# Kernel optimization log

Hardware: AMD Instinct MI355X
Metric: run time of the kernel (lower is better)

The kernel has to match this reference:

```python
import jax, jax.numpy as jnp
import numpy as np

VOCAB, INPUT, HIDDEN, OUT = 100000, 256, 512, 5
BATCH, SEQ = 64, 512

def _xavier(key, shape):
    fan_in, fan_out = shape[1], shape[0]
    limit = float(np.sqrt(6.0 / (fan_in + fan_out)))
    return jax.random.uniform(key, shape, jnp.float32, -limit, limit)

def setup_inputs() -> dict:
    key = jax.random.key(0)
    ks = jax.random.split(key, 5)
    x = jax.random.randint(ks[0], (BATCH, SEQ), 0, VOCAB)
    embedding = _xavier(ks[1], (VOCAB, INPUT))
    embedding = embedding.at[0].set(0.0)  # padding_idx=0
    W_ih = _xavier(ks[2], (4 * HIDDEN, INPUT))
    b_ih = jnp.zeros((4 * HIDDEN,), jnp.float32)
    W_hh = _xavier(ks[3], (4 * HIDDEN, HIDDEN))
    b_hh = jnp.zeros((4 * HIDDEN,), jnp.float32)
    W_out = _xavier(ks[4], (OUT, HIDDEN))
    b_out = jnp.zeros((OUT,), jnp.float32)
    return {"x": x, "embedding": embedding, "W_ih": W_ih, "b_ih": b_ih,
            "W_hh": W_hh, "b_hh": b_hh, "W_out": W_out, "b_out": b_out}

def reference(x, embedding, W_ih, b_ih, W_hh, b_hh, W_out, b_out):
    bs = x.shape[0]
    HS = W_hh.shape[1]
    # embedding lookup for all timesteps; padding_idx=0 rows are zero
    emb = embedding[x]                                   # [B, S, INPUT]
    emb = jnp.where((x == 0)[..., None], 0.0, emb)
    # input-to-hidden projection is time-independent: hoist out of the recurrence
    x_proj = jnp.einsum('bsi,gi->bsg', emb, W_ih) + b_ih + b_hh  # [B, S, 4H]

    def step(carry, xp_t):
        h, c = carry
        gates = xp_t + h @ W_hh.T                        # [B, 4H]
        i = jax.nn.sigmoid(gates[:, :HS])
        f = jax.nn.sigmoid(gates[:, HS:2 * HS])
        g = jnp.tanh(gates[:, 2 * HS:3 * HS])
        o = jax.nn.sigmoid(gates[:, 3 * HS:])
        c = f * c + i * g
        h = o * jnp.tanh(c)
        return (h, c), None

    h0 = jnp.zeros((bs, HS), x_proj.dtype)
    c0 = jnp.zeros((bs, HS), x_proj.dtype)
    (h_t, c_t), _ = jax.lax.scan(step, (h0, c0), jnp.swapaxes(x_proj, 0, 1))
    out = h_t @ W_out.T + b_out                          # [B, OUT]
    return out, (h_t, c_t)
```

## Files before the change

kernel.cpp:

```cpp
#include <hip/hip_runtime.h>
#include <stdint.h>

typedef unsigned short u16;
typedef uint32_t u32;
typedef __attribute__((ext_vector_type(4))) u32 u32x4;
typedef __attribute__((ext_vector_type(8))) short v8s;
typedef __attribute__((ext_vector_type(4))) float f32x4;

#define OFF_H  0
#define OFF_WF 262144

__device__ __forceinline__ u16 bf_hi(float v) {
  return (u16)(__builtin_bit_cast(u32, v) >> 16);
}
__device__ __forceinline__ float bf_up(u16 h) {
  return __builtin_bit_cast(float, (u32)h << 16);
}
__device__ __forceinline__ float tanhf_fast(float x) {
  float e = __expf(2.f * x);
  return 1.f - 2.f / (e + 1.f);
}
__device__ __forceinline__ float sigm(float x) {
  return 1.f / (1.f + __expf(-x));
}
__device__ __forceinline__ u32 pkhi(u32 a, u32 b) { return __builtin_amdgcn_perm(b, a, 0x07060302u); }
__device__ __forceinline__ u32 pklo(u32 a, u32 b) { return __builtin_amdgcn_perm(b, a, 0x05040100u); }

__global__ void k_init(u32* h) {
  int i = blockIdx.x * 256 + threadIdx.x;
  if (i < 65536) h[i] = (i < 32768) ? 0u : 1u;
}

__global__ void k_prep(const float* __restrict__ Wih, const float* __restrict__ Whh,
                       u16* __restrict__ wf) {
  int idx = blockIdx.x * 256 + threadIdx.x;
  if (idx >= 64 * 2 * 24 * 64) return;
  int lane = idx & 63;
  int r1 = idx >> 6;
  int c  = r1 % 24;
  int r2 = r1 / 24;
  int nt = r2 & 1;
  int wg = r2 >> 1;
  int n32 = nt * 16 + (lane & 15);
  int R = (n32 >> 3) * 512 + wg * 8 + (n32 & 7);
  int gq = lane >> 4;
  const float* src = (c < 8) ? (Wih + (size_t)R * 256 + c * 32 + 8 * gq)
                             : (Whh + (size_t)R * 512 + (c - 8) * 32 + 8 * gq);
  u16* d = wf + (size_t)idx * 16;
#pragma unroll
  for (int i = 0; i < 8; ++i) {
    float v = src[i];
    u16 hi = bf_hi(v);
    float lo = v - bf_up(hi);
    d[i] = hi;
    d[8 + i] = bf_hi(lo);
  }
}

#define LOADP(DST, PTR) \
  asm volatile("global_load_dwordx4 %0, %1, off" : "=v"(DST) : "v"(PTR))
#define LOADC(DST, PTR) \
  asm volatile("global_load_dwordx4 %0, %1, off sc0 sc1" : "=v"(DST) : "v"(PTR))
#define STORED(PTR, VAL) \
  asm volatile("global_store_dword %0, %1, off sc0 sc1" :: "v"(PTR), "v"(VAL) : "memory")

#define WAITV_(N) { asm volatile("s_waitcnt vmcnt(" #N ")" ::: "memory"); \
                    __builtin_amdgcn_sched_barrier(0); }
#define WAITV(N) WAITV_(N)

#define MFMA16(a, b, c) __builtin_amdgcn_mfma_f32_16x16x32_bf16((a), (b), (c), 0, 0, 0)
#define BC(x) __builtin_bit_cast(v8s, x)

#define MM6(AH, AL, B) { \
  v8s b0h_ = BC((B)[0]), b0l_ = BC((B)[1]), b1h_ = BC((B)[2]), b1l_ = BC((B)[3]); \
  acc[0] = MFMA16((AH), b0h_, acc[0]); \
  acc[0] = MFMA16((AH), b0l_, acc[0]); \
  acc[0] = MFMA16((AL), b0h_, acc[0]); \
  acc[1] = MFMA16((AH), b1h_, acc[1]); \
  acc[1] = MFMA16((AH), b1l_, acc[1]); \
  acc[1] = MFMA16((AL), b1h_, acc[1]); }

#define TAGOK(j) (__all((( (HA[2*(j)][0]^texp) | (HA[2*(j)][1]^texp) \
                         | (HA[2*(j)][2]^texp) | (HA[2*(j)][3]^texp) \
                         | (HA[2*(j)+1][0]^texp) | (HA[2*(j)+1][1]^texp) \
                         | (HA[2*(j)+1][2]^texp) | (HA[2*(j)+1][3]^texp)) & 1u) == 0u))

#define CONSJ(j) { \
  u32x4 w0 = HA[2*(j)], w1 = HA[2*(j)+1]; \
  u32x4 hiw, low; \
  hiw[0] = pkhi(w0[0], w0[1]); hiw[1] = pkhi(w0[2], w0[3]); \
  hiw[2] = pkhi(w1[0], w1[1]); hiw[3] = pkhi(w1[2], w1[3]); \
  low[0] = pklo(w0[0], w0[1]); low[1] = pklo(w0[2], w0[3]); \
  low[2] = pklo(w1[0], w1[1]); low[3] = pklo(w1[2], w1[3]); \
  v8s ah = BC(hiw), al = BC(low); \
  MM6(ah, al, BH[j]); }

#define ISSUEJ(j) { LOADC(HA[2*(j)], pp[j]); LOADC(HA[2*(j)+1], pp[j] + 4); }
#define RISS(c)  if (pend & (1u<<(c))) ISSUEJ(c)
#define RCON(c)  if (pend & (1u<<(c))) { if (TAGOK(c)) { CONSJ(c); pend &= ~(1u<<(c)); } }

__global__ __launch_bounds__(256, 1) void k_lstm(
    const int* __restrict__ xin, const float* __restrict__ emb,
    const float* __restrict__ bih, const float* __restrict__ bhh,
    uint8_t* __restrict__ ws, float* __restrict__ dout)
{
  const int bid = blockIdx.x;
  const int wg = bid & 63;
  const int g  = bid >> 6;
  const int tid = threadIdx.x;
  const int wv = tid >> 6;
  const int lane = tid & 63;
  const int cl = lane & 15;
  const int gq = lane >> 4;

  u32* hbuf = (u32*)(ws + OFF_H);
  const u16* wf = (const u16*)(ws + OFF_WF);

  __shared__ f32x4 red[2][4][2][64];

  float bias[2];
#pragma unroll
  for (int nt = 0; nt < 2; ++nt) {
    int n32 = nt * 16 + cl;
    int R = (n32 >> 3) * 512 + wg * 8 + (n32 & 7);
    bias[nt] = bih[R] + bhh[R];
  }

  u32x4 BH[4][4], WB[2][4];
#pragma unroll
  for (int j = 0; j < 4; ++j) {
    const u32x4* p0 = (const u32x4*)(wf + ((((size_t)wg*2+0)*24 + (8 + wv + 4*j))*64 + lane)*16);
    const u32x4* p1 = (const u32x4*)(wf + ((((size_t)wg*2+1)*24 + (8 + wv + 4*j))*64 + lane)*16);
    BH[j][0] = p0[0]; BH[j][1] = p0[1];
    BH[j][2] = p1[0]; BH[j][3] = p1[1];
  }
#pragma unroll
  for (int J = 0; J < 2; ++J) {
    const u32x4* p0 = (const u32x4*)(wf + ((((size_t)wg*2+0)*24 + (4*J + wv))*64 + lane)*16);
    const u32x4* p1 = (const u32x4*)(wf + ((((size_t)wg*2+1)*24 + (4*J + wv))*64 + lane)*16);
    WB[J][0] = p0[0]; WB[J][1] = p0[1];
    WB[J][2] = p1[0]; WB[J][3] = p1[1];
  }

  const int brow = g * 16 + cl;
  const int koA = wv * 32 + 8 * gq;
  const int koB = (4 + wv) * 32 + 8 * gq;

  u32x4 EA[4];
  {
    int tok0 = xin[brow * 512];
    const float* eb = emb + (size_t)tok0 * 256;
    LOADP(EA[0], eb + koA); LOADP(EA[1], eb + koA + 4);
    LOADP(EA[2], eb + koB); LOADP(EA[3], eb + koB + 4);
  }
  WAITV(0);

  float cst[4] = {0.f, 0.f, 0.f, 0.f};
  int delay = 16;

  for (int t = 0; t < 512; ++t) {
    const u32* hc = hbuf + ((size_t)(t & 1) * 4 + g) * 8192;
    u32* hn = hbuf + ((size_t)((t + 1) & 1) * 4 + g) * 8192;
    const u32 texp = (u32)((t >> 1) & 1);
    const u32* pp[4];
    pp[0] = hc + cl * 512 + (wv + 0) * 32 + 8 * gq;
    pp[1] = hc + cl * 512 + (wv + 4) * 32 + 8 * gq;
    pp[2] = hc + cl * 512 + (wv + 8) * 32 + 8 * gq;
    pp[3] = hc + cl * 512 + (wv + 12) * 32 + 8 * gq;

    for (int d = delay; d > 0; --d) __builtin_amdgcn_s_sleep(1);

    int tok;
    asm volatile("global_load_dword %0, %1, off"
                 : "=v"(tok) : "v"(xin + brow * 512 + ((t + 1) & 511)));
    u32x4 HA[8];
    ISSUEJ(0); ISSUEJ(1); ISSUEJ(2); ISSUEJ(3);
    __builtin_amdgcn_sched_barrier(0);

    WAITV(13);
    f32x4 acc[2] = {};
    {
      u32x4 h0, h1;
      h0[0] = pkhi(EA[0][0], EA[0][1]); h0[1] = pkhi(EA[0][2], EA[0][3]);
      h0[2] = pkhi(EA[1][0], EA[1][1]); h0[3] = pkhi(EA[1][2], EA[1][3]);
      h1[0] = pkhi(EA[2][0], EA[2][1]); h1[1] = pkhi(EA[2][2], EA[2][3]);
      h1[2] = pkhi(EA[3][0], EA[3][1]); h1[3] = pkhi(EA[3][2], EA[3][3]);
      v8s a0 = BC(h0), a1 = BC(h1);
      acc[0] = MFMA16(a0, BC(WB[0][0]), acc[0]);
      acc[0] = MFMA16(a0, BC(WB[0][1]), acc[0]);
      acc[1] = MFMA16(a0, BC(WB[0][2]), acc[1]);
      acc[1] = MFMA16(a0, BC(WB[0][3]), acc[1]);
      acc[0] = MFMA16(a1, BC(WB[1][0]), acc[0]);
      acc[0] = MFMA16(a1, BC(WB[1][1]), acc[0]);
      acc[1] = MFMA16(a1, BC(WB[1][2]), acc[1]);
      acc[1] = MFMA16(a1, BC(WB[1][3]), acc[1]);
    }

    u32 pend = 0;
    WAITV(6); if (TAGOK(0)) { CONSJ(0); } else pend |= 1u;
    WAITV(4); if (TAGOK(1)) { CONSJ(1); } else pend |= 2u;
    WAITV(2); if (TAGOK(2)) { CONSJ(2); } else pend |= 4u;
    WAITV(0); if (TAGOK(3)) { CONSJ(3); } else pend |= 8u;

    delay = pend ? ((delay > 56) ? 64 : delay + 8) : ((delay > 0) ? delay - 1 : 0);

    int fuse = 0;
    while (pend) {
      __builtin_amdgcn_s_sleep(1);
      RISS(0); RISS(1); RISS(2); RISS(3);
      WAITV(0);
      RCON(0); RCON(1); RCON(2); RCON(3);
      if (++fuse > 16384) break;
    }
    asm volatile("s_waitcnt vmcnt(0)" : "+v"(tok) :: "memory");
    __builtin_amdgcn_sched_barrier(0);

    red[t & 1][wv][0][lane] = acc[0];
    red[t & 1][wv][1][lane] = acc[1];
    __syncthreads();

    {
      const float* eb = emb + (size_t)(u32)tok * 256;
      LOADP(EA[0], eb + koA); LOADP(EA[1], eb + koA + 4);
      LOADP(EA[2], eb + koB); LOADP(EA[3], eb + koB + 4);
    }

    f32x4 fin0 = red[t & 1][0][0][lane] + red[t & 1][1][0][lane]
               + red[t & 1][2][0][lane] + red[t & 1][3][0][lane];
    f32x4 fin1 = red[t & 1][0][1][lane] + red[t & 1][1][1][lane]
               + red[t & 1][2][1][lane] + red[t & 1][3][1][lane];
    fin0 += bias[0];
    fin1 += bias[1];

    const u32 tagn = (u32)(((t + 1) >> 1) & 1);
#pragma unroll
    for (int r = 0; r < 4; ++r) {
      float iv = fin0[r];
      float gv = fin1[r];
      float fv = __shfl_xor(iv, 8, 64);
      float ov = __shfl_xor(gv, 8, 64);
      float ii = sigm(iv);
      float ff = sigm(fv);
      float gg = tanhf_fast(gv);
      float oo = sigm(ov);
      float cn = ff * cst[r] + ii * gg;
      cst[r] = cn;
      float hnv = oo * tanhf_fast(cn);
      if (gq == wv && cl < 8) {
        int row = 4 * gq + r;
        int jj = wg * 8 + cl;
        if (t < 511) {
          u16 hi = bf_hi(hnv);
          u16 lo = bf_hi(hnv - bf_up(hi));
          u32 word = ((u32)hi << 16) | ((u32)lo & 0xfffeu) | tagn;
          STORED(hn + row * 512 + jj, word);
        } else {
          int b = g * 16 + row;
          dout[320 + b * 512 + jj] = hnv;
          dout[320 + 32768 + b * 512 + jj] = cn;
        }
      }
    }
  }
}

__global__ void k_out(const float* __restrict__ Wout, const float* __restrict__ bout,
                      float* __restrict__ dout) {
  int i = threadIdx.x;
  if (i >= 320) return;
  int b = i / 5, o = i - b * 5;
  const float* hp = dout + 320 + b * 512;
  const float* wp = Wout + (size_t)o * 512;
  float s = 0.f;
#pragma unroll 4
  for (int k = 0; k < 512; k += 4) {
    s += hp[k] * wp[k] + hp[k + 1] * wp[k + 1] + hp[k + 2] * wp[k + 2] + hp[k + 3] * wp[k + 3];
  }
  dout[i] = s + bout[o];
}

extern "C" void kernel_launch(void* const* d_in, const int* in_sizes, int n_in,
                              void* d_out, int out_size, void* d_ws, size_t ws_size,
                              hipStream_t stream) {
  const int* x = (const int*)d_in[0];
  const float* emb = (const float*)d_in[1];
  const float* Wih = (const float*)d_in[2];
  const float* bih = (const float*)d_in[3];
  const float* Whh = (const float*)d_in[4];
  const float* bhh = (const float*)d_in[5];
  const float* Wout = (const float*)d_in[6];
  const float* bout = (const float*)d_in[7];
  float* out = (float*)d_out;
  uint8_t* ws = (uint8_t*)d_ws;

  hipLaunchKernelGGL(k_init, dim3(256), dim3(256), 0, stream, (u32*)ws);
  hipLaunchKernelGGL(k_prep, dim3(768), dim3(256), 0, stream, Wih, Whh, (u16*)(ws + OFF_WF));
  hipLaunchKernelGGL(k_lstm, dim3(256), dim3(256), 0, stream, x, emb, bih, bhh, ws, out);
  hipLaunchKernelGGL(k_out, dim3(1), dim3(320), 0, stream, Wout, bout, out);
}
```

Before: 1.702 ms.

## Halve LSTM workgroups to 128, each owning 16 hidden units, and hoist input MFMAs

Repartitions the persistent LSTM so each workgroup computes 16 hidden units (four 16-column gate tiles) instead of 8, halving the grid from 256 to 128 blocks and the number of participants in the cross-block h exchange. The weight-prep layout, bias indexing, reduction buffer and h-store ownership are rewritten to match. The input-projection MFMAs now run before the spin delay and the recurrent h loads, overlapping them with the wait. In exchange, each wave holds twice the register-resident weights and does twice the MFMA work per step, which lengthens per-step compute and raises register pressure.

```diff
diff --git a/kernel.cpp b/kernel.cpp
--- a/kernel.cpp
+++ b/kernel.cpp
@@ -34,15 +34,17 @@
 __global__ void k_prep(const float* __restrict__ Wih, const float* __restrict__ Whh,
                        u16* __restrict__ wf) {
   int idx = blockIdx.x * 256 + threadIdx.x;
-  if (idx >= 64 * 2 * 24 * 64) return;
+  if (idx >= 196608) return;
   int lane = idx & 63;
-  int r1 = idx >> 6;
-  int c  = r1 % 24;
-  int r2 = r1 / 24;
-  int nt = r2 & 1;
-  int wg = r2 >> 1;
-  int n32 = nt * 16 + (lane & 15);
-  int R = (n32 >> 3) * 512 + wg * 8 + (n32 & 7);
+  int c  = (idx >> 6) % 24;
+  int r2 = (idx >> 6) / 24;
+  int nt = r2 & 3;
+  int wg = r2 >> 2;
+  int n16 = lane & 15;
+  int h = nt >> 1, t2 = nt & 1;
+  int q = t2 * 2 + (n16 >> 3);
+  int u = h * 8 + (n16 & 7);
+  int R = q * 512 + wg * 16 + u;
   int gq = lane >> 4;
   const float* src = (c < 8) ? (Wih + (size_t)R * 256 + c * 32 + 8 * gq)
                              : (Whh + (size_t)R * 512 + (c - 8) * 32 + 8 * gq);
@@ -71,14 +73,11 @@
 #define MFMA16(a, b, c) __builtin_amdgcn_mfma_f32_16x16x32_bf16((a), (b), (c), 0, 0, 0)
 #define BC(x) __builtin_bit_cast(v8s, x)
 
-#define MM6(AH, AL, B) { \
-  v8s b0h_ = BC((B)[0]), b0l_ = BC((B)[1]), b1h_ = BC((B)[2]), b1l_ = BC((B)[3]); \
-  acc[0] = MFMA16((AH), b0h_, acc[0]); \
-  acc[0] = MFMA16((AH), b0l_, acc[0]); \
-  acc[0] = MFMA16((AL), b0h_, acc[0]); \
-  acc[1] = MFMA16((AH), b1h_, acc[1]); \
-  acc[1] = MFMA16((AH), b1l_, acc[1]); \
-  acc[1] = MFMA16((AL), b1h_, acc[1]); }
+#define MM3(AH, AL, BHI, BLO, ACC) { \
+  v8s bh_ = BC(BHI), bl_ = BC(BLO); \
+  (ACC) = MFMA16((AH), bh_, (ACC)); \
+  (ACC) = MFMA16((AH), bl_, (ACC)); \
+  (ACC) = MFMA16((AL), bh_, (ACC)); }
 
 #define TAGOK(j) (__all((( (HA[2*(j)][0]^texp) | (HA[2*(j)][1]^texp) \
                          | (HA[2*(j)][2]^texp) | (HA[2*(j)][3]^texp) \
@@ -93,7 +92,10 @@
   low[0] = pklo(w0[0], w0[1]); low[1] = pklo(w0[2], w0[3]); \
   low[2] = pklo(w1[0], w1[1]); low[3] = pklo(w1[2], w1[3]); \
   v8s ah = BC(hiw), al = BC(low); \
-  MM6(ah, al, BH[j]); }
+  MM3(ah, al, BH[j][0], BH[j][1], acc[0]); \
+  MM3(ah, al, BH[j][2], BH[j][3], acc[1]); \
+  MM3(ah, al, BH[j][4], BH[j][5], acc[2]); \
+  MM3(ah, al, BH[j][6], BH[j][7], acc[3]); }
 
 #define ISSUEJ(j) { LOADC(HA[2*(j)], pp[j]); LOADC(HA[2*(j)+1], pp[j] + 4); }
 #define RISS(c)  if (pend & (1u<<(c))) ISSUEJ(c)
@@ -105,42 +107,46 @@
     uint8_t* __restrict__ ws, float* __restrict__ dout)
 {
   const int bid = blockIdx.x;
-  const int wg = bid & 63;
-  const int g  = bid >> 6;
+  const int wg = bid & 31;
+  const int g  = bid >> 5;
   const int tid = threadIdx.x;
   const int wv = tid >> 6;
   const int lane = tid & 63;
   const int cl = lane & 15;
   const int gq = lane >> 4;
+  const int hb = wv >> 1;
 
   u32* hbuf = (u32*)(ws + OFF_H);
   const u16* wf = (const u16*)(ws + OFF_WF);
 
-  __shared__ f32x4 red[2][4][2][64];
+  __shared__ f32x4 red[2][4][4][64];
 
   float bias[2];
-#pragma unroll
-  for (int nt = 0; nt < 2; ++nt) {
-    int n32 = nt * 16 + cl;
-    int R = (n32 >> 3) * 512 + wg * 8 + (n32 & 7);
-    bias[nt] = bih[R] + bhh[R];
-  }
-
-  u32x4 BH[4][4], WB[2][4];
-#pragma unroll
-  for (int j = 0; j < 4; ++j) {
-    const u32x4* p0 = (const u32x4*)(wf + ((((size_t)wg*2+0)*24 + (8 + wv + 4*j))*64 + lane)*16);
-    const u32x4* p1 = (const u32x4*)(wf + ((((size_t)wg*2+1)*24 + (8 + wv + 4*j))*64 + lane)*16);
-    BH[j][0] = p0[0]; BH[j][1] = p0[1];
-    BH[j][2] = p1[0]; BH[j][3] = p1[1];
-  }
-#pragma unroll
-  for (int J = 0; J < 2; ++J) {
-    const u32x4* p0 = (const u32x4*)(wf + ((((size_t)wg*2+0)*24 + (4*J + wv))*64 + lane)*16);
-    const u32x4* p1 = (const u32x4*)(wf + ((((size_t)wg*2+1)*24 + (4*J + wv))*64 + lane)*16);
-    WB[J][0] = p0[0]; WB[J][1] = p0[1];
-    WB[J][2] = p1[0]; WB[J][3] = p1[1];
-  }
+  {
+    int u7 = cl & 7;
+    int R0 = (cl >> 3) * 512 + wg * 16 + hb * 8 + u7;
+    int R1 = (2 + (cl >> 3)) * 512 + wg * 16 + hb * 8 + u7;
+    bias[0] = bih[R0] + bhh[R0];
+    bias[1] = bih[R1] + bhh[R1];
+  }
+
+  u32x4 BH[4][8], WB[2][8];
+#pragma unroll
+  for (int j = 0; j < 4; ++j)
+#pragma unroll
+    for (int nt = 0; nt < 4; ++nt) {
+      const u32x4* p = (const u32x4*)(wf + ((((size_t)wg*4 + nt)*24 + (8 + wv + 4*j))*64 + lane)*16);
+      BH[j][2*nt]   = p[0];
+      BH[j][2*nt+1] = p[1];
+    }
+#pragma unroll
+  for (int J = 0; J < 2; ++J)
+#pragma unroll
+    for (int nt = 0; nt < 4; ++nt) {
+      const u32x4* p = (const u32x4*)(wf + ((((size_t)wg*4 + nt)*24 + (4*J + wv))*64 + lane)*16);
+      WB[J][2*nt]   = p[0];
+      WB[J][2*nt+1] = p[1];
+    }
 
   const int brow = g * 16 + cl;
   const int koA = wv * 32 + 8 * gq;
@@ -168,17 +174,8 @@
     pp[2] = hc + cl * 512 + (wv + 8) * 32 + 8 * gq;
     pp[3] = hc + cl * 512 + (wv + 12) * 32 + 8 * gq;
 
-    for (int d = delay; d > 0; --d) __builtin_amdgcn_s_sleep(1);
-
-    int tok;
-    asm volatile("global_load_dword %0, %1, off"
-                 : "=v"(tok) : "v"(xin + brow * 512 + ((t + 1) & 511)));
-    u32x4 HA[8];
-    ISSUEJ(0); ISSUEJ(1); ISSUEJ(2); ISSUEJ(3);
-    __builtin_amdgcn_sched_barrier(0);
-
-    WAITV(13);
-    f32x4 acc[2] = {};
+    WAITV(4);
+    f32x4 acc[4] = {};
     {
       u32x4 h0, h1;
       h0[0] = pkhi(EA[0][0], EA[0][1]); h0[1] = pkhi(EA[0][2], EA[0][3]);
@@ -186,15 +183,23 @@
       h1[0] = pkhi(EA[2][0], EA[2][1]); h1[1] = pkhi(EA[2][2], EA[2][3]);
       h1[2] = pkhi(EA[3][0], EA[3][1]); h1[3] = pkhi(EA[3][2], EA[3][3]);
       v8s a0 = BC(h0), a1 = BC(h1);
-      acc[0] = MFMA16(a0, BC(WB[0][0]), acc[0]);
-      acc[0] = MFMA16(a0, BC(WB[0][1]), acc[0]);
-      acc[1] = MFMA16(a0, BC(WB[0][2]), acc[1]);
-      acc[1] = MFMA16(a0, BC(WB[0][3]), acc[1]);
-      acc[0] = MFMA16(a1, BC(WB[1][0]), acc[0]);
-      acc[0] = MFMA16(a1, BC(WB[1][1]), acc[0]);
-      acc[1] = MFMA16(a1, BC(WB[1][2]), acc[1]);
-      acc[1] = MFMA16(a1, BC(WB[1][3]), acc[1]);
-    }
+#pragma unroll
+      for (int nt = 0; nt < 4; ++nt) {
+        acc[nt] = MFMA16(a0, BC(WB[0][2*nt]),   acc[nt]);
+        acc[nt] = MFMA16(a0, BC(WB[0][2*nt+1]), acc[nt]);
+        acc[nt] = MFMA16(a1, BC(WB[1][2*nt]),   acc[nt]);
+        acc[nt] = MFMA16(a1, BC(WB[1][2*nt+1]), acc[nt]);
+      }
+    }
+
+    for (int d = delay; d > 0; --d) __builtin_amdgcn_s_sleep(1);
+
+    int tok;
+    asm volatile("global_load_dword %0, %1, off"
+                 : "=v"(tok) : "v"(xin + brow * 512 + ((t + 1) & 511)));
+    u32x4 HA[8];
+    ISSUEJ(0); ISSUEJ(1); ISSUEJ(2); ISSUEJ(3);
+    __builtin_amdgcn_sched_barrier(0);
 
     u32 pend = 0;
     WAITV(6); if (TAGOK(0)) { CONSJ(0); } else pend |= 1u;
@@ -215,8 +220,8 @@
     asm volatile("s_waitcnt vmcnt(0)" : "+v"(tok) :: "memory");
     __builtin_amdgcn_sched_barrier(0);
 
-    red[t & 1][wv][0][lane] = acc[0];
-    red[t & 1][wv][1][lane] = acc[1];
+#pragma unroll
+    for (int nt = 0; nt < 4; ++nt) red[t & 1][wv][nt][lane] = acc[nt];
     __syncthreads();
 
     {
@@ -225,10 +230,11 @@
       LOADP(EA[2], eb + koB); LOADP(EA[3], eb + koB + 4);
     }
 
-    f32x4 fin0 = red[t & 1][0][0][lane] + red[t & 1][1][0][lane]
-               + red[t & 1][2][0][lane] + red[t & 1][3][0][lane];
-    f32x4 fin1 = red[t & 1][0][1][lane] + red[t & 1][1][1][lane]
-               + red[t & 1][2][1][lane] + red[t & 1][3][1][lane];
+    const int n0 = hb * 2;
+    f32x4 fin0 = red[t & 1][0][n0][lane] + red[t & 1][1][n0][lane]
+               + red[t & 1][2][n0][lane] + red[t & 1][3][n0][lane];
+    f32x4 fin1 = red[t & 1][0][n0+1][lane] + red[t & 1][1][n0+1][lane]
+               + red[t & 1][2][n0+1][lane] + red[t & 1][3][n0+1][lane];
     fin0 += bias[0];
     fin1 += bias[1];
 
@@ -246,9 +252,9 @@
       float cn = ff * cst[r] + ii * gg;
       cst[r] = cn;
       float hnv = oo * tanhf_fast(cn);
-      if (gq == wv && cl < 8) {
+      if (((gq ^ wv) & 1) == 0 && cl < 8) {
         int row = 4 * gq + r;
-        int jj = wg * 8 + cl;
+        int jj = wg * 16 + hb * 8 + cl;
         if (t < 511) {
           u16 hi = bf_hi(hnv);
           u16 lo = bf_hi(hnv - bf_up(hi));
@@ -295,6 +301,6 @@
 
   hipLaunchKernelGGL(k_init, dim3(256), dim3(256), 0, stream, (u32*)ws);
   hipLaunchKernelGGL(k_prep, dim3(768), dim3(256), 0, stream, Wih, Whh, (u16*)(ws + OFF_WF));
-  hipLaunchKernelGGL(k_lstm, dim3(256), dim3(256), 0, stream, x, emb, bih, bhh, ws, out);
+  hipLaunchKernelGGL(k_lstm, dim3(128), dim3(256), 0, stream, x, emb, bih, bhh, ws, out);
   hipLaunchKernelGGL(k_out, dim3(1), dim3(320), 0, stream, Wout, bout, out);
 }
```

New measurement: 1.778 ms. 4.4% more time.
